# Performance work log

Measured on AMD Instinct MI355X. Metric: run time of the kernel, lower is better.

The kernel has to match this reference:

```python
import jax, jax.numpy as jnp
import numpy as np
from jax import lax


def _bayer_kernels():
    # 5 fixed 3x3 interpolation stencils (identity, plus-avg, cross-avg, h-avg, v-avg)
    k5 = np.array([
        [[0, 0, 0], [0, 1, 0], [0, 0, 0]],
        [[0, .25, 0], [.25, 0, .25], [0, .25, 0]],
        [[.25, 0, .25], [0, 0, 0], [.25, 0, .25]],
        [[0, 0, 0], [.5, 0, .5], [0, 0, 0]],
        [[0, .5, 0], [0, 0, 0], [0, .5, 0]],
    ], dtype=np.float32)  # (5,3,3)
    # 4 fixed (3,5) selection matrices (1x1 convs per Bayer quadrant)
    sel = np.array([
        [[0, 0, 1, 0, 0], [0, 1, 0, 0, 0], [1, 0, 0, 0, 0]],
        [[0, 0, 0, 0, 1], [1, 0, 0, 0, 0], [0, 0, 0, 1, 0]],
        [[0, 0, 0, 1, 0], [1, 0, 0, 0, 0], [0, 0, 0, 0, 1]],
        [[1, 0, 0, 0, 0], [0, 1, 0, 0, 0], [0, 0, 1, 0, 0]],
    ], dtype=np.float32)  # (4,3,5)
    return jnp.asarray(k5), jnp.asarray(sel)


def setup_inputs() -> dict:
    key = jax.random.key(0)
    x = jax.random.uniform(key, (2, 1, 4096, 4096), dtype=jnp.float32) * 255.0
    k5, sel = _bayer_kernels()
    return {"x": x, "kernels5": k5, "sel": sel}


def reference(x, kernels5, sel):
    n, _, h, w = x.shape
    x_pad = jnp.pad(x, ((0, 0), (0, 0), (1, 1), (1, 1)), mode="reflect")
    # 3x3 stencil bank: (N,1,H+2,W+2) -> (N,5,H,W)
    xc = lax.conv_general_dilated(
        x_pad, kernels5.reshape(5, 1, 3, 3), window_strides=(1, 1),
        padding="VALID", dimension_numbers=("NCHW", "OIHW", "NCHW"))
    h2, w2 = h // 2, w // 2
    # pixel-unshuffle (DCR order): (N,5,H,W) -> (N, 2,2, 5, H/2, W/2) -> (N,4,5,H/2,W/2)
    u = xc.reshape(n, 5, h2, 2, w2, 2).transpose(0, 3, 5, 1, 2, 4).reshape(n, 4, 5, h2, w2)
    # per-quadrant 1x1 selection conv: (N,4,3,H/2,W/2)
    e = jnp.einsum("qos,nqsxy->nqoxy", sel, u)
    # pixel-shuffle (DCR order): (N,4,3,H/2,W/2) -> (N,3,H,W)
    y = e.reshape(n, 2, 2, 3, h2, w2).transpose(0, 3, 4, 1, 5, 2).reshape(n, 3, h, w)
    return y
```

## Files before the change

### kernel.cpp

```cpp
#include <hip/hip_runtime.h>


#define IMG_H 4096
#define IMG_W 4096
#define T_PAIRS 4

typedef float v4f __attribute__((ext_vector_type(4)));

__device__ __forceinline__ void load_win(const float* __restrict__ rowp, int j,
                                         int lane, float w[6]) {
    const float4 v = *(const float4*)(rowp + j);
    w[1] = v.x; w[2] = v.y; w[3] = v.z; w[4] = v.w;
    float left  = __shfl_up(v.w, 1);
    float right = __shfl_down(v.x, 1);
    if (lane == 0)  left  = (j == 0) ? v.y : rowp[j - 1];
    if (lane == 63) right = (j == IMG_W - 4) ? v.z : rowp[j + 4];
    w[0] = left; w[5] = right;
}

__global__ __launch_bounds__(256) void bayer_demosaic_kernel(
    const float* __restrict__ x, float* __restrict__ out) {
    const int jg   = blockIdx.x * blockDim.x + threadIdx.x;
    const int j    = jg << 2;
    const int lane = threadIdx.x & 63;
    const int n    = blockIdx.z;
    int r = blockIdx.y * (2 * T_PAIRS);

    const float* xn = x + (size_t)n * IMG_H * IMG_W;
    float* on       = out + (size_t)n * 3 * IMG_H * IMG_W;
    const size_t plane = (size_t)IMG_H * IMG_W;

    float A[6], B[6], C[6], D[6];
    {
        const int rm = (r == 0) ? 1 : r - 1;
        load_win(xn + (size_t)rm * IMG_W, j, lane, A);
        load_win(xn + (size_t)r  * IMG_W, j, lane, B);
    }

#pragma unroll
    for (int t = 0; t < T_PAIRS; ++t, r += 2) {
        const int rp = (r == IMG_H - 2) ? IMG_H - 2 : r + 2;
        load_win(xn + (size_t)(r + 1) * IMG_W, j, lane, C);
        load_win(xn + (size_t)rp * IMG_W, j, lane, D);

        float e0[4], e1[4], e2[4];
        float f0[4], f1[4], f2[4];
#pragma unroll
        for (int k = 0; k < 4; ++k) {
            {
                const float center = B[k + 1];
                const float plus   = 0.25f * (A[k + 1] + C[k + 1] + B[k] + B[k + 2]);
                const float cross  = 0.25f * (A[k] + A[k + 2] + C[k] + C[k + 2]);
                const float havg   = 0.5f  * (B[k] + B[k + 2]);
                const float vavg   = 0.5f  * (A[k + 1] + C[k + 1]);
                if ((k & 1) == 0) { e0[k] = cross; e1[k] = plus;   e2[k] = center; }
                else              { e0[k] = vavg;  e1[k] = center; e2[k] = havg;   }
            }
            {
                const float center = C[k + 1];
                const float plus   = 0.25f * (B[k + 1] + D[k + 1] + C[k] + C[k + 2]);
                const float cross  = 0.25f * (B[k] + B[k + 2] + D[k] + D[k + 2]);
                const float havg   = 0.5f  * (C[k] + C[k + 2]);
                const float vavg   = 0.5f  * (B[k + 1] + D[k + 1]);
                if ((k & 1) == 0) { f0[k] = havg;   f1[k] = center; f2[k] = vavg;  }
                else              { f0[k] = center; f1[k] = plus;   f2[k] = cross; }
            }
        }

        const size_t off0 = (size_t)r * IMG_W + j;
        const size_t off1 = off0 + IMG_W;
        v4f s;
        s = (v4f){e0[0], e0[1], e0[2], e0[3]};
        __builtin_nontemporal_store(s, (v4f*)(on + off0));
        s = (v4f){f0[0], f0[1], f0[2], f0[3]};
        __builtin_nontemporal_store(s, (v4f*)(on + off1));
        s = (v4f){e1[0], e1[1], e1[2], e1[3]};
        __builtin_nontemporal_store(s, (v4f*)(on + plane + off0));
        s = (v4f){f1[0], f1[1], f1[2], f1[3]};
        __builtin_nontemporal_store(s, (v4f*)(on + plane + off1));
        s = (v4f){e2[0], e2[1], e2[2], e2[3]};
        __builtin_nontemporal_store(s, (v4f*)(on + 2 * plane + off0));
        s = (v4f){f2[0], f2[1], f2[2], f2[3]};
        __builtin_nontemporal_store(s, (v4f*)(on + 2 * plane + off1));

#pragma unroll
        for (int q = 0; q < 6; ++q) { A[q] = C[q]; B[q] = D[q]; }
    }
}

extern "C" void kernel_launch(void* const* d_in, const int* in_sizes, int n_in,
                              void* d_out, int out_size, void* d_ws, size_t ws_size,
                              hipStream_t stream) {
    const float* x = (const float*)d_in[0];
    float* out = (float*)d_out;

    const int N = 2;
    dim3 block(256, 1, 1);
    dim3 grid(IMG_W / 4 / 256, IMG_H / (2 * T_PAIRS), N);
    bayer_demosaic_kernel<<<grid, block, 0, stream>>>(x, out);
}
```

Measured before the change: 498.2 us.

## Widen thread tile to eight columns and drop vertical row-pair loop

Each thread now processes eight columns and a single Bayer row pair, instead of four columns across four consecutive row pairs. All four needed input rows are loaded up front with two float4 loads each, and the grid is reshaped to twice as many blocks. The intent is more independent loads in flight per thread and more blocks to hide memory latency. In exchange, vertical row reuse between row pairs is lost, so each input row is read about twice, relying on cache to absorb it.

```diff
diff --git a/kernel.cpp b/kernel.cpp
--- a/kernel.cpp
+++ b/kernel.cpp
@@ -3,88 +3,98 @@
 
 #define IMG_H 4096
 #define IMG_W 4096
-#define T_PAIRS 4
 
 typedef float v4f __attribute__((ext_vector_type(4)));
 
-__device__ __forceinline__ void load_win(const float* __restrict__ rowp, int j,
-                                         int lane, float w[6]) {
-    const float4 v = *(const float4*)(rowp + j);
-    w[1] = v.x; w[2] = v.y; w[3] = v.z; w[4] = v.w;
-    float left  = __shfl_up(v.w, 1);
-    float right = __shfl_down(v.x, 1);
-    if (lane == 0)  left  = (j == 0) ? v.y : rowp[j - 1];
-    if (lane == 63) right = (j == IMG_W - 4) ? v.z : rowp[j + 4];
-    w[0] = left; w[5] = right;
+__device__ __forceinline__ void load_win8(const float* __restrict__ rowp, int j,
+                                          int lane, float w[10]) {
+    const float4 v0 = *(const float4*)(rowp + j);
+    const float4 v1 = *(const float4*)(rowp + j + 4);
+    w[1] = v0.x; w[2] = v0.y; w[3] = v0.z; w[4] = v0.w;
+    w[5] = v1.x; w[6] = v1.y; w[7] = v1.z; w[8] = v1.w;
+    float left  = __shfl_up(v1.w, 1);
+    float right = __shfl_down(v0.x, 1);
+    if (lane == 0)  left  = (j == 0) ? v0.y : rowp[j - 1];
+    if (lane == 63) right = (j == IMG_W - 8) ? v1.z : rowp[j + 8];
+    w[0] = left; w[9] = right;
 }
 
 __global__ __launch_bounds__(256) void bayer_demosaic_kernel(
     const float* __restrict__ x, float* __restrict__ out) {
     const int jg   = blockIdx.x * blockDim.x + threadIdx.x;
-    const int j    = jg << 2;
+    const int j    = jg << 3;
     const int lane = threadIdx.x & 63;
     const int n    = blockIdx.z;
-    int r = blockIdx.y * (2 * T_PAIRS);
+    const int r    = blockIdx.y << 1;
 
     const float* xn = x + (size_t)n * IMG_H * IMG_W;
     float* on       = out + (size_t)n * 3 * IMG_H * IMG_W;
     const size_t plane = (size_t)IMG_H * IMG_W;
 
-    float A[6], B[6], C[6], D[6];
+    const int rm = (r == 0) ? 1 : r - 1;
+    const int rp = (r == IMG_H - 2) ? IMG_H - 2 : r + 2;
+
+    float A[10], B[10], C[10], D[10];
+    load_win8(xn + (size_t)rm * IMG_W, j, lane, A);
+    load_win8(xn + (size_t)r  * IMG_W, j, lane, B);
+    load_win8(xn + (size_t)(r + 1) * IMG_W, j, lane, C);
+    load_win8(xn + (size_t)rp * IMG_W, j, lane, D);
+
+    const size_t off0 = (size_t)r * IMG_W + j;
+    const size_t off1 = off0 + IMG_W;
+
     {
-        const int rm = (r == 0) ? 1 : r - 1;
-        load_win(xn + (size_t)rm * IMG_W, j, lane, A);
-        load_win(xn + (size_t)r  * IMG_W, j, lane, B);
+        float o0[8], o1[8], o2[8];
+#pragma unroll
+        for (int k = 0; k < 8; ++k) {
+            const float center = B[k + 1];
+            const float plus   = 0.25f * (A[k + 1] + C[k + 1] + B[k] + B[k + 2]);
+            const float cross  = 0.25f * (A[k] + A[k + 2] + C[k] + C[k + 2]);
+            const float havg   = 0.5f  * (B[k] + B[k + 2]);
+            const float vavg   = 0.5f  * (A[k + 1] + C[k + 1]);
+            if ((k & 1) == 0) { o0[k] = cross; o1[k] = plus;   o2[k] = center; }
+            else              { o0[k] = vavg;  o1[k] = center; o2[k] = havg;   }
+        }
+        v4f s;
+        s = (v4f){o0[0], o0[1], o0[2], o0[3]};
+        __builtin_nontemporal_store(s, (v4f*)(on + off0));
+        s = (v4f){o0[4], o0[5], o0[6], o0[7]};
+        __builtin_nontemporal_store(s, (v4f*)(on + off0 + 4));
+        s = (v4f){o1[0], o1[1], o1[2], o1[3]};
+        __builtin_nontemporal_store(s, (v4f*)(on + plane + off0));
+        s = (v4f){o1[4], o1[5], o1[6], o1[7]};
+        __builtin_nontemporal_store(s, (v4f*)(on + plane + off0 + 4));
+        s = (v4f){o2[0], o2[1], o2[2], o2[3]};
+        __builtin_nontemporal_store(s, (v4f*)(on + 2 * plane + off0));
+        s = (v4f){o2[4], o2[5], o2[6], o2[7]};
+        __builtin_nontemporal_store(s, (v4f*)(on + 2 * plane + off0 + 4));
     }
 
+    {
+        float o0[8], o1[8], o2[8];
 #pragma unroll
-    for (int t = 0; t < T_PAIRS; ++t, r += 2) {
-        const int rp = (r == IMG_H - 2) ? IMG_H - 2 : r + 2;
-        load_win(xn + (size_t)(r + 1) * IMG_W, j, lane, C);
-        load_win(xn + (size_t)rp * IMG_W, j, lane, D);
-
-        float e0[4], e1[4], e2[4];
-        float f0[4], f1[4], f2[4];
-#pragma unroll
-        for (int k = 0; k < 4; ++k) {
-            {
-                const float center = B[k + 1];
-                const float plus   = 0.25f * (A[k + 1] + C[k + 1] + B[k] + B[k + 2]);
-                const float cross  = 0.25f * (A[k] + A[k + 2] + C[k] + C[k + 2]);
-                const float havg   = 0.5f  * (B[k] + B[k + 2]);
-                const float vavg   = 0.5f  * (A[k + 1] + C[k + 1]);
-                if ((k & 1) == 0) { e0[k] = cross; e1[k] = plus;   e2[k] = center; }
-                else              { e0[k] = vavg;  e1[k] = center; e2[k] = havg;   }
-            }
-            {
-                const float center = C[k + 1];
-                const float plus   = 0.25f * (B[k + 1] + D[k + 1] + C[k] + C[k + 2]);
-                const float cross  = 0.25f * (B[k] + B[k + 2] + D[k] + D[k + 2]);
-                const float havg   = 0.5f  * (C[k] + C[k + 2]);
-                const float vavg   = 0.5f  * (B[k + 1] + D[k + 1]);
-                if ((k & 1) == 0) { f0[k] = havg;   f1[k] = center; f2[k] = vavg;  }
-                else              { f0[k] = center; f1[k] = plus;   f2[k] = cross; }
-            }
+        for (int k = 0; k < 8; ++k) {
+            const float center = C[k + 1];
+            const float plus   = 0.25f * (B[k + 1] + D[k + 1] + C[k] + C[k + 2]);
+            const float cross  = 0.25f * (B[k] + B[k + 2] + D[k] + D[k + 2]);
+            const float havg   = 0.5f  * (C[k] + C[k + 2]);
+            const float vavg   = 0.5f  * (B[k + 1] + D[k + 1]);
+            if ((k & 1) == 0) { o0[k] = havg;   o1[k] = center; o2[k] = vavg;  }
+            else              { o0[k] = center; o1[k] = plus;   o2[k] = cross; }
         }
-
-        const size_t off0 = (size_t)r * IMG_W + j;
-        const size_t off1 = off0 + IMG_W;
         v4f s;
-        s = (v4f){e0[0], e0[1], e0[2], e0[3]};
-        __builtin_nontemporal_store(s, (v4f*)(on + off0));
-        s = (v4f){f0[0], f0[1], f0[2], f0[3]};
+        s = (v4f){o0[0], o0[1], o0[2], o0[3]};
         __builtin_nontemporal_store(s, (v4f*)(on + off1));
-        s = (v4f){e1[0], e1[1], e1[2], e1[3]};
-        __builtin_nontemporal_store(s, (v4f*)(on + plane + off0));
-        s = (v4f){f1[0], f1[1], f1[2], f1[3]};
+        s = (v4f){o0[4], o0[5], o0[6], o0[7]};
+        __builtin_nontemporal_store(s, (v4f*)(on + off1 + 4));
+        s = (v4f){o1[0], o1[1], o1[2], o1[3]};
         __builtin_nontemporal_store(s, (v4f*)(on + plane + off1));
-        s = (v4f){e2[0], e2[1], e2[2], e2[3]};
-        __builtin_nontemporal_store(s, (v4f*)(on + 2 * plane + off0));
-        s = (v4f){f2[0], f2[1], f2[2], f2[3]};
+        s = (v4f){o1[4], o1[5], o1[6], o1[7]};
+        __builtin_nontemporal_store(s, (v4f*)(on + plane + off1 + 4));
+        s = (v4f){o2[0], o2[1], o2[2], o2[3]};
         __builtin_nontemporal_store(s, (v4f*)(on + 2 * plane + off1));
-
-#pragma unroll
-        for (int q = 0; q < 6; ++q) { A[q] = C[q]; B[q] = D[q]; }
+        s = (v4f){o2[4], o2[5], o2[6], o2[7]};
+        __builtin_nontemporal_store(s, (v4f*)(on + 2 * plane + off1 + 4));
     }
 }
 
@@ -96,6 +106,6 @@
 
     const int N = 2;
     dim3 block(256, 1, 1);
-    dim3 grid(IMG_W / 4 / 256, IMG_H / (2 * T_PAIRS), N);
+    dim3 grid(IMG_W / 8 / 256, IMG_H / 2, N);
     bayer_demosaic_kernel<<<grid, block, 0, stream>>>(x, out);
 }
```

Result: slower. 614.2 us (+23.3%).
